# Performance work log

Hardware: AMD Instinct MI355X
Metric: run time of the kernel (lower is better)

## Reference

```python
import jax, jax.numpy as jnp
import numpy as np

DIM = 2048
N_HEADS = 16
HEAD_DIM = 128
EPS = 1e-6


def setup_inputs() -> dict:
    key = jax.random.key(0)
    ks = jax.random.split(key, 8)
    b, gf, gh, gw = 1, 8, 16, 24
    s = gf * gh * gw
    c = HEAD_DIM // 2
    w = lambda k: 0.02 * jax.random.normal(k, (DIM, DIM), jnp.float32)
    return {
        "x": jax.random.normal(ks[0], (b, s, DIM), jnp.float32),
        "freqs_angle": jax.random.normal(ks[1], (1024, c), jnp.float32),
        "Wq": w(ks[2]), "bq": jnp.zeros((DIM,), jnp.float32),
        "Wk": w(ks[3]), "bk": jnp.zeros((DIM,), jnp.float32),
        "Wv": w(ks[4]), "bv": jnp.zeros((DIM,), jnp.float32),
        "Wo": w(ks[5]), "bo": jnp.zeros((DIM,), jnp.float32),
        "gq": jnp.ones((DIM,), jnp.float32),
        "gk": jnp.ones((DIM,), jnp.float32),
        "seq_len": s, "grid_f": gf, "grid_h": gh, "grid_w": gw,
    }


def _rms(t, g):
    return t * jax.lax.rsqrt(jnp.mean(t * t, axis=-1, keepdims=True) + EPS) * g


def _grid_angles(freqs_angle, gf, gh, gw, c):
    # band split [c - 2*(c//3), c//3, c//3] as in rope_apply
    cf = c - 2 * (c // 3)
    ch = cw = c // 3
    af = freqs_angle[:gf, :cf]            # [F, cf]
    ah = freqs_angle[:gh, cf:cf + ch]     # [H, ch]
    aw = freqs_angle[:gw, cf + ch:c]      # [W, cw]
    ang = jnp.concatenate([
        jnp.broadcast_to(af[:, None, None, :], (gf, gh, gw, cf)),
        jnp.broadcast_to(ah[None, :, None, :], (gf, gh, gw, ch)),
        jnp.broadcast_to(aw[None, None, :, :], (gf, gh, gw, cw)),
    ], axis=-1)
    return ang.reshape(gf * gh * gw, c)   # [s, c]


def reference(x, freqs_angle, Wq, bq, Wk, bk, Wv, bv, Wo, bo, gq, gk,
              seq_len, grid_f, grid_h, grid_w):
    b, s, _ = x.shape
    n, d = N_HEADS, HEAD_DIM
    c = d // 2
    ang = _grid_angles(freqs_angle, grid_f, grid_h, grid_w, c)
    cos = jnp.cos(ang)[None, :, None, :]  # [1, s, 1, c]
    sin = jnp.sin(ang)[None, :, None, :]

    def rope(t):  # complex multiply on (even, odd) = (real, imag) pairs
        te, to = t[..., 0::2], t[..., 1::2]
        return jnp.stack([te * cos - to * sin, te * sin + to * cos], axis=-1).reshape(t.shape)

    q = _rms(x @ Wq.T + bq, gq).reshape(b, s, n, d)
    k = _rms(x @ Wk.T + bk, gk).reshape(b, s, n, d)
    v = (x @ Wv.T + bv).reshape(b, s, n, d)
    q, k = rope(q), rope(k)

    scale = np.float32(1.0 / np.sqrt(d))
    scores = jnp.einsum('bqnd,bknd->bnqk', q, k) * scale
    p = jax.nn.softmax(scores, axis=-1)
    o = jnp.einsum('bnqk,bknd->bqnd', p, v).reshape(b, s, n * d)
    return o @ Wo.T + bo
```

## Files before the change

kernel.cpp:

```cpp
#include <hip/hip_runtime.h>
#include <stdint.h>
#include <stddef.h>

typedef __bf16 bf16_t;
typedef __bf16 bf16x8 __attribute__((ext_vector_type(8)));
typedef __bf16 bf16x4 __attribute__((ext_vector_type(4)));
typedef __bf16 bf16x2 __attribute__((ext_vector_type(2)));
typedef float  f32x4  __attribute__((ext_vector_type(4)));

#define SEQ   3072
#define DIMD  2048
#define NH    16
#define HD    128
#define QKVN  6144

__device__ __forceinline__ void async16(const bf16_t* g, bf16_t* l) {
  __builtin_amdgcn_global_load_lds((const __attribute__((address_space(1))) uint32_t*)g,
                                   (__attribute__((address_space(3))) uint32_t*)l, 16, 0, 0);
}

__global__ __launch_bounds__(256) void cvt_all(const float* __restrict__ x,
                                               const float* __restrict__ Wq,
                                               const float* __restrict__ Wk,
                                               const float* __restrict__ Wv,
                                               const float* __restrict__ Wo,
                                               const float* __restrict__ bq,
                                               const float* __restrict__ bk,
                                               const float* __restrict__ bv,
                                               bf16_t* __restrict__ xb,
                                               bf16_t* __restrict__ Wqkvb,
                                               bf16_t* __restrict__ Wob,
                                               float* __restrict__ bqkv) {
  const int b = blockIdx.x;
  const float* src; bf16_t* dst; int off;
  if (b < 3072)       { src = x;  dst = xb;              off = b; }
  else if (b < 5120)  { src = Wq; dst = Wqkvb;           off = b - 3072; }
  else if (b < 7168)  { src = Wk; dst = Wqkvb + 4194304; off = b - 5120; }
  else if (b < 9216)  { src = Wv; dst = Wqkvb + 8388608; off = b - 7168; }
  else if (b < 11264) { src = Wo; dst = Wob;             off = b - 9216; }
  else {
    int t = (b - 11264) * 256 + threadIdx.x;
    float v;
    if (t < 2048)      v = bq[t];
    else if (t < 4096) v = bk[t - 2048];
    else               v = bv[t - 4096];
    bqkv[t] = v;
    return;
  }
  const int idx = (off * 256 + threadIdx.x) * 8;
  const float4 a = *(const float4*)(src + idx);
  const float4 c = *(const float4*)(src + idx + 4);
  bf16x8 o;
  o[0] = (bf16_t)a.x; o[1] = (bf16_t)a.y; o[2] = (bf16_t)a.z; o[3] = (bf16_t)a.w;
  o[4] = (bf16_t)c.x; o[5] = (bf16_t)c.y; o[6] = (bf16_t)c.z; o[7] = (bf16_t)c.w;
  *(bf16x8*)(dst + idx) = o;
}

template<bool OUT_BF16>
__global__ __launch_bounds__(256, 2) void gemm_nt(const bf16_t* __restrict__ A,
                                                  const bf16_t* __restrict__ B,
                                                  const float* __restrict__ bias,
                                                  void* __restrict__ Cout,
                                                  int M, int N, int K) {
  __shared__ __align__(16) bf16_t As[128 * 64];
  __shared__ __align__(16) bf16_t Bs[128 * 64];
  const int t = threadIdx.x;
  const int lane = t & 63, wave = t >> 6;
  const int quad = lane >> 4, l15 = lane & 15;
  const int wy = wave >> 1, wx = wave & 1;
  const size_t bm = (size_t)blockIdx.y * 128, bn = (size_t)blockIdx.x * 128;
  const bf16_t* Ab = A + bm * K;
  const bf16_t* Bb = B + bn * K;
  f32x4 acc[4][4] = {};
  int srow[4], scol[4];
#pragma unroll
  for (int r = 0; r < 4; r++) {
    int L = r * 256 + t;
    int row = L >> 3, cp = L & 7;
    srow[r] = row;
    scol[r] = (cp ^ (row & 7)) * 8;
  }
  for (int k0 = 0; k0 < K; k0 += 64) {
    __syncthreads();
#pragma unroll
    for (int r = 0; r < 4; r++)
      async16(Ab + (size_t)srow[r] * K + k0 + scol[r], &As[(r * 256 + t) * 8]);
#pragma unroll
    for (int r = 0; r < 4; r++)
      async16(Bb + (size_t)srow[r] * K + k0 + scol[r], &Bs[(r * 256 + t) * 8]);
    __syncthreads();
#pragma unroll
    for (int ks = 0; ks < 2; ks++) {
      bf16x8 af[4], bfv[4];
#pragma unroll
      for (int i = 0; i < 4; i++) {
        int row = wy * 64 + i * 16 + l15;
        af[i] = *(const bf16x8*)&As[row * 64 + (((ks * 4 + quad) ^ (row & 7)) * 8)];
      }
#pragma unroll
      for (int j = 0; j < 4; j++) {
        int row = wx * 64 + j * 16 + l15;
        bfv[j] = *(const bf16x8*)&Bs[row * 64 + (((ks * 4 + quad) ^ (row & 7)) * 8)];
      }
#pragma unroll
      for (int i = 0; i < 4; i++)
#pragma unroll
        for (int j = 0; j < 4; j++)
          acc[i][j] = __builtin_amdgcn_mfma_f32_16x16x32_bf16(af[i], bfv[j], acc[i][j], 0, 0, 0);
    }
  }
#pragma unroll
  for (int i = 0; i < 4; i++) {
#pragma unroll
    for (int j = 0; j < 4; j++) {
      size_t row = bm + wy * 64 + i * 16 + quad * 4;
      size_t col = bn + wx * 64 + j * 16 + l15;
      float bb = bias[col];
#pragma unroll
      for (int r = 0; r < 4; r++) {
        float v = acc[i][j][r] + bb;
        if (OUT_BF16) ((bf16_t*)Cout)[(row + r) * N + col] = (bf16_t)v;
        else          ((float*)Cout)[(row + r) * N + col] = v;
      }
    }
  }
}

__global__ __launch_bounds__(256) void rmsrope(bf16_t* __restrict__ qkv,
                                               bf16_t* __restrict__ pk,
                                               const float* __restrict__ gq,
                                               const float* __restrict__ gk,
                                               const float* __restrict__ freqs) {
  const int s = blockIdx.x, t = threadIdx.x;
  bf16_t* row = qkv + (size_t)s * QKVN;
  bf16x8 qv = *(const bf16x8*)&row[t * 8];
  bf16x8 kv = *(const bf16x8*)&row[2048 + t * 8];
  float qf[8], kf[8];
  float qs = 0.f, ks2 = 0.f;
#pragma unroll
  for (int i = 0; i < 8; i++) {
    qf[i] = (float)qv[i]; qs  += qf[i] * qf[i];
    kf[i] = (float)kv[i]; ks2 += kf[i] * kf[i];
  }
#pragma unroll
  for (int m = 1; m < 64; m <<= 1) {
    qs  += __shfl_xor(qs, m);
    ks2 += __shfl_xor(ks2, m);
  }
  __shared__ float red[2][4];
  const int wave = t >> 6, lane = t & 63;
  if (lane == 0) { red[0][wave] = qs; red[1][wave] = ks2; }
  __syncthreads();
  qs  = red[0][0] + red[0][1] + red[0][2] + red[0][3];
  ks2 = red[1][0] + red[1][1] + red[1][2] + red[1][3];
  const float qsc = rsqrtf(qs  / 2048.f + 1e-6f);
  const float ksc = rsqrtf(ks2 / 2048.f + 1e-6f);
  const int sf = s / 384, rem = s - sf * 384;
  const int sh = rem / 24, sw = rem - sh * 24;
  bf16x8 qo, ko;
#pragma unroll
  for (int u = 0; u < 4; u++) {
    const int col = t * 8 + 2 * u;
    const int i = (col >> 1) & 63;
    const int frow = (i < 22) ? sf : ((i < 43) ? sh : sw);
    const float ang = freqs[frow * 64 + i];
    float sn, cs;
    __sincosf(ang, &sn, &cs);
    float te = qf[2 * u]     * qsc * gq[col];
    float to = qf[2 * u + 1] * qsc * gq[col + 1];
    qo[2 * u]     = (bf16_t)(te * cs - to * sn);
    qo[2 * u + 1] = (bf16_t)(te * sn + to * cs);
    te = kf[2 * u]     * ksc * gk[col];
    to = kf[2 * u + 1] * ksc * gk[col + 1];
    ko[2 * u]     = (bf16_t)(te * cs - to * sn);
    ko[2 * u + 1] = (bf16_t)(te * sn + to * cs);
  }
  *(bf16x8*)&row[t * 8] = qo;
  *(bf16x8*)&pk[((size_t)(t >> 4) * SEQ + s) * HD + (t & 15) * 8] = ko;
}

__global__ __launch_bounds__(256) void vtrans(const bf16_t* __restrict__ qkv,
                                              bf16_t* __restrict__ pvt) {
  __shared__ bf16_t tile[128][65];
  const int h = blockIdx.y;
  const int s0 = blockIdx.x * 64;
  const int t = threadIdx.x;
#pragma unroll
  for (int r = 0; r < 4; r++) {
    int L = r * 256 + t, s = L >> 4, cp = L & 15;
    bf16x8 v = *(const bf16x8*)&qkv[(size_t)(s0 + s) * QKVN + 4096 + h * HD + cp * 8];
#pragma unroll
    for (int i = 0; i < 8; i++) tile[cp * 8 + i][s] = v[i];
  }
  __syncthreads();
#pragma unroll
  for (int r = 0; r < 4; r++) {
    int L = r * 256 + t, d = L >> 3, c = L & 7;
    bf16x8 o;
#pragma unroll
    for (int i = 0; i < 8; i++) o[i] = tile[d][c * 8 + i];
    *(bf16x8*)&pvt[((size_t)h * HD + d) * SEQ + s0 + c * 8] = o;
  }
}

__global__ __launch_bounds__(256, 2) void flash_attn(const bf16_t* __restrict__ qkv,
                                                     const bf16_t* __restrict__ pk,
                                                     const bf16_t* __restrict__ pvt,
                                                     bf16_t* __restrict__ ob) {
  __shared__ __align__(16) bf16_t Ks[2][64 * 128];
  __shared__ __align__(16) bf16_t Vt[2][128 * 64];
  __shared__ __align__(16) bf16_t Ps[4][32 * 64];
  const int h = blockIdx.y, qt = blockIdx.x;
  const int s0 = qt * 128;
  const int t = threadIdx.x, wave = t >> 6, lane = t & 63;
  const int quad = lane >> 4, l15 = lane & 15;
  const int wq = wave * 32;
  const float scale = 0.08838834764831845f;
  const bf16_t* pkh = pk  + (size_t)h * (SEQ * HD);
  const bf16_t* pvh = pvt + (size_t)h * (HD * SEQ);
  int krow4[4], kc4[4], vd4[4], vc4[4];
#pragma unroll
  for (int r = 0; r < 4; r++) {
    int L = r * 256 + t;
    krow4[r] = L >> 4; kc4[r] = (L & 15) ^ (krow4[r] & 7);
    vd4[r]   = L >> 3; vc4[r] = (L & 7)  ^ (vd4[r] & 7);
  }
  bf16x8 qfr[2][4];
#pragma unroll
  for (int tj = 0; tj < 2; tj++)
#pragma unroll
    for (int ks = 0; ks < 4; ks++)
      qfr[tj][ks] = *(const bf16x8*)&qkv[(size_t)(s0 + wq + tj * 16 + l15) * QKVN + h * HD + ks * 32 + quad * 8];
  f32x4 oacc[2][8] = {};
  float m_run[2] = {-3e38f, -3e38f}, l_run[2] = {0.f, 0.f};
#pragma unroll
  for (int r = 0; r < 4; r++) {
    int L = r * 256 + t;
    async16(pkh + (size_t)krow4[r] * HD + kc4[r] * 8, &Ks[0][L * 8]);
  }
#pragma unroll
  for (int r = 0; r < 4; r++) {
    int L = r * 256 + t;
    async16(pvh + (size_t)vd4[r] * SEQ + vc4[r] * 8, &Vt[0][L * 8]);
  }
  for (int kt = 0; kt < SEQ / 64; kt++) {
    const int cur = kt & 1;
    __syncthreads();
    if (kt + 1 < SEQ / 64) {
      const int kv1 = (kt + 1) * 64;
#pragma unroll
      for (int r = 0; r < 4; r++) {
        int L = r * 256 + t;
        async16(pkh + (size_t)(kv1 + krow4[r]) * HD + kc4[r] * 8, &Ks[cur ^ 1][L * 8]);
      }
#pragma unroll
      for (int r = 0; r < 4; r++) {
        int L = r * 256 + t;
        async16(pvh + (size_t)vd4[r] * SEQ + kv1 + vc4[r] * 8, &Vt[cur ^ 1][L * 8]);
      }
    }
    f32x4 st[4][2] = {};
#pragma unroll
    for (int ks = 0; ks < 4; ks++) {
      bf16x8 kfr[4];
#pragma unroll
      for (int ti = 0; ti < 4; ti++) {
        const int kr = ti * 16 + l15;
        kfr[ti] = *(const bf16x8*)&Ks[cur][kr * 128 + (((ks * 4 + quad) ^ (kr & 7)) * 8)];
      }
#pragma unroll
      for (int ti = 0; ti < 4; ti++)
#pragma unroll
        for (int tj = 0; tj < 2; tj++)
          st[ti][tj] = __builtin_amdgcn_mfma_f32_16x16x32_bf16(kfr[ti], qfr[tj][ks], st[ti][tj], 0, 0, 0);
    }
    float mt[2] = {-3e38f, -3e38f};
#pragma unroll
    for (int ti = 0; ti < 4; ti++)
#pragma unroll
      for (int tj = 0; tj < 2; tj++)
#pragma unroll
        for (int r = 0; r < 4; r++) {
          st[ti][tj][r] *= scale;
          mt[tj] = fmaxf(mt[tj], st[ti][tj][r]);
        }
    float al[2];
#pragma unroll
    for (int tj = 0; tj < 2; tj++) {
      mt[tj] = fmaxf(mt[tj], __shfl_xor(mt[tj], 16));
      mt[tj] = fmaxf(mt[tj], __shfl_xor(mt[tj], 32));
      const float mn = fmaxf(m_run[tj], mt[tj]);
      al[tj] = __expf(m_run[tj] - mn);
      m_run[tj] = mn;
    }
    float lt[2] = {0.f, 0.f};
#pragma unroll
    for (int ti = 0; ti < 4; ti++)
#pragma unroll
      for (int tj = 0; tj < 2; tj++) {
        bf16x4 pv;
#pragma unroll
        for (int r = 0; r < 4; r++) {
          const float p = __expf(st[ti][tj][r] - m_run[tj]);
          pv[r] = (bf16_t)p;
          lt[tj] += (float)pv[r];
        }
        const int q = tj * 16 + l15;
        const int cp2 = (ti * 2 + (quad >> 1)) ^ (q & 7);
        *(bf16x4*)&Ps[wave][q * 64 + cp2 * 8 + (quad & 1) * 4] = pv;
      }
#pragma unroll
    for (int tj = 0; tj < 2; tj++) {
      lt[tj] += __shfl_xor(lt[tj], 16);
      lt[tj] += __shfl_xor(lt[tj], 32);
      l_run[tj] = l_run[tj] * al[tj] + lt[tj];
    }
#pragma unroll
    for (int ti = 0; ti < 2; ti++) {
      float a0 = __shfl(al[ti], quad * 4 + 0);
      float a1 = __shfl(al[ti], quad * 4 + 1);
      float a2 = __shfl(al[ti], quad * 4 + 2);
      float a3 = __shfl(al[ti], quad * 4 + 3);
#pragma unroll
      for (int dj = 0; dj < 8; dj++) {
        oacc[ti][dj][0] *= a0; oacc[ti][dj][1] *= a1;
        oacc[ti][dj][2] *= a2; oacc[ti][dj][3] *= a3;
      }
    }
#pragma unroll
    for (int ks = 0; ks < 2; ks++) {
      bf16x8 pf[2], vf[8];
#pragma unroll
      for (int ti = 0; ti < 2; ti++) {
        const int q = ti * 16 + l15;
        pf[ti] = *(const bf16x8*)&Ps[wave][q * 64 + (((ks * 4 + quad) ^ (q & 7)) * 8)];
      }
#pragma unroll
      for (int dj = 0; dj < 8; dj++) {
        const int d = dj * 16 + l15;
        vf[dj] = *(const bf16x8*)&Vt[cur][d * 64 + (((ks * 4 + quad) ^ (d & 7)) * 8)];
      }
#pragma unroll
      for (int ti = 0; ti < 2; ti++)
#pragma unroll
        for (int dj = 0; dj < 8; dj++)
          oacc[ti][dj] = __builtin_amdgcn_mfma_f32_16x16x32_bf16(pf[ti], vf[dj], oacc[ti][dj], 0, 0, 0);
    }
  }
#pragma unroll
  for (int ti = 0; ti < 2; ti++) {
    float li[4];
#pragma unroll
    for (int r = 0; r < 4; r++) li[r] = 1.f / __shfl(l_run[ti], quad * 4 + r);
#pragma unroll
    for (int dj = 0; dj < 8; dj++)
#pragma unroll
      for (int r = 0; r < 4; r++) {
        const float v = oacc[ti][dj][r] * li[r];
        ob[(size_t)(s0 + wq + ti * 16 + quad * 4 + r) * DIMD + h * HD + dj * 16 + l15] = (bf16_t)v;
      }
  }
}

extern "C" void kernel_launch(void* const* d_in, const int* in_sizes, int n_in,
                              void* d_out, int out_size, void* d_ws, size_t ws_size,
                              hipStream_t stream) {
  (void)in_sizes; (void)n_in; (void)out_size;
  const float* x     = (const float*)d_in[0];
  const float* freqs = (const float*)d_in[1];
  const float* Wq    = (const float*)d_in[2];
  const float* bq    = (const float*)d_in[3];
  const float* Wk    = (const float*)d_in[4];
  const float* bk    = (const float*)d_in[5];
  const float* Wv    = (const float*)d_in[6];
  const float* bv    = (const float*)d_in[7];
  const float* Wo    = (const float*)d_in[8];
  const float* bo    = (const float*)d_in[9];
  const float* gq    = (const float*)d_in[10];
  const float* gk    = (const float*)d_in[11];

  char* w = (char*)d_ws;
  bf16_t* xb    = (bf16_t*)(w);
  bf16_t* Wqkvb = (bf16_t*)(w + 12582912);
  bf16_t* Wob   = (bf16_t*)(w + 37748736);
  bf16_t* qkvb  = (bf16_t*)(w + 46137344);
  bf16_t* obuf  = (bf16_t*)(w + 83886080);
  float*  bqkv  = (float*) (w + 96468992);
  bf16_t* pk    = (bf16_t*)(w);
  bf16_t* pvt   = (bf16_t*)(w + 12582912);
  if (ws_size < (size_t)96493568) return;

  cvt_all<<<11288, 256, 0, stream>>>(x, Wq, Wk, Wv, Wo, bq, bk, bv, xb, Wqkvb, Wob, bqkv);

  gemm_nt<true><<<dim3(48, 24), 256, 0, stream>>>(xb, Wqkvb, bqkv, qkvb, SEQ, QKVN, DIMD);
  rmsrope<<<3072, 256, 0, stream>>>(qkvb, pk, gq, gk, freqs);
  vtrans<<<dim3(48, NH), 256, 0, stream>>>(qkvb, pvt);
  flash_attn<<<dim3(24, NH), 256, 0, stream>>>(qkvb, pk, pvt, obuf);
  gemm_nt<false><<<dim3(16, 24), 256, 0, stream>>>(obuf, Wob, bo, (float*)d_out, SEQ, DIMD, DIMD);
}
```

Measured before the change: 421.5 us.

## Widen flash-attention blocks to six waves, use exp2 softmax, skip unneeded rescale

The flash attention kernel now runs 384 threads (six waves) per block, each block covering 192 query rows. The grid shrinks to 16x16 blocks, so each K/V tile loaded into LDS serves more queries. The softmax folds log2(e) into the scale and uses exp2f, and the accumulator rescale is skipped when no lane's correction factor differs from one. The grid becomes 256 blocks with one block per CU under the new launch bounds, which may reduce latency hiding and leave some CUs idle. The K/V load loops no longer divide evenly across threads.

```diff
diff --git a/kernel.cpp b/kernel.cpp
--- a/kernel.cpp
+++ b/kernel.cpp
@@ -203,28 +203,21 @@
   }
 }
 
-__global__ __launch_bounds__(256, 2) void flash_attn(const bf16_t* __restrict__ qkv,
+__global__ __launch_bounds__(384, 1) void flash_attn(const bf16_t* __restrict__ qkv,
                                                      const bf16_t* __restrict__ pk,
                                                      const bf16_t* __restrict__ pvt,
                                                      bf16_t* __restrict__ ob) {
   __shared__ __align__(16) bf16_t Ks[2][64 * 128];
   __shared__ __align__(16) bf16_t Vt[2][128 * 64];
-  __shared__ __align__(16) bf16_t Ps[4][32 * 64];
+  __shared__ __align__(16) bf16_t Ps[6][32 * 64];
   const int h = blockIdx.y, qt = blockIdx.x;
-  const int s0 = qt * 128;
+  const int s0 = qt * 192;
   const int t = threadIdx.x, wave = t >> 6, lane = t & 63;
   const int quad = lane >> 4, l15 = lane & 15;
   const int wq = wave * 32;
-  const float scale = 0.08838834764831845f;
+  const float scale2 = 0.08838834764831845f * 1.44269504088896f;
   const bf16_t* pkh = pk  + (size_t)h * (SEQ * HD);
   const bf16_t* pvh = pvt + (size_t)h * (HD * SEQ);
-  int krow4[4], kc4[4], vd4[4], vc4[4];
-#pragma unroll
-  for (int r = 0; r < 4; r++) {
-    int L = r * 256 + t;
-    krow4[r] = L >> 4; kc4[r] = (L & 15) ^ (krow4[r] & 7);
-    vd4[r]   = L >> 3; vc4[r] = (L & 7)  ^ (vd4[r] & 7);
-  }
   bf16x8 qfr[2][4];
 #pragma unroll
   for (int tj = 0; tj < 2; tj++)
@@ -233,30 +226,26 @@
       qfr[tj][ks] = *(const bf16x8*)&qkv[(size_t)(s0 + wq + tj * 16 + l15) * QKVN + h * HD + ks * 32 + quad * 8];
   f32x4 oacc[2][8] = {};
   float m_run[2] = {-3e38f, -3e38f}, l_run[2] = {0.f, 0.f};
-#pragma unroll
-  for (int r = 0; r < 4; r++) {
-    int L = r * 256 + t;
-    async16(pkh + (size_t)krow4[r] * HD + kc4[r] * 8, &Ks[0][L * 8]);
-  }
-#pragma unroll
-  for (int r = 0; r < 4; r++) {
-    int L = r * 256 + t;
-    async16(pvh + (size_t)vd4[r] * SEQ + vc4[r] * 8, &Vt[0][L * 8]);
+  for (int L = t; L < 1024; L += 384) {
+    int krow = L >> 4, c = (L & 15) ^ (krow & 7);
+    async16(pkh + (size_t)krow * HD + c * 8, &Ks[0][L * 8]);
+  }
+  for (int L = t; L < 1024; L += 384) {
+    int d = L >> 3, c = (L & 7) ^ (d & 7);
+    async16(pvh + (size_t)d * SEQ + c * 8, &Vt[0][L * 8]);
   }
   for (int kt = 0; kt < SEQ / 64; kt++) {
     const int cur = kt & 1;
     __syncthreads();
     if (kt + 1 < SEQ / 64) {
       const int kv1 = (kt + 1) * 64;
-#pragma unroll
-      for (int r = 0; r < 4; r++) {
-        int L = r * 256 + t;
-        async16(pkh + (size_t)(kv1 + krow4[r]) * HD + kc4[r] * 8, &Ks[cur ^ 1][L * 8]);
-      }
-#pragma unroll
-      for (int r = 0; r < 4; r++) {
-        int L = r * 256 + t;
-        async16(pvh + (size_t)vd4[r] * SEQ + kv1 + vc4[r] * 8, &Vt[cur ^ 1][L * 8]);
+      for (int L = t; L < 1024; L += 384) {
+        int krow = L >> 4, c = (L & 15) ^ (krow & 7);
+        async16(pkh + (size_t)(kv1 + krow) * HD + c * 8, &Ks[cur ^ 1][L * 8]);
+      }
+      for (int L = t; L < 1024; L += 384) {
+        int d = L >> 3, c = (L & 7) ^ (d & 7);
+        async16(pvh + (size_t)d * SEQ + kv1 + c * 8, &Vt[cur ^ 1][L * 8]);
       }
     }
     f32x4 st[4][2] = {};
@@ -281,7 +270,7 @@
       for (int tj = 0; tj < 2; tj++)
 #pragma unroll
         for (int r = 0; r < 4; r++) {
-          st[ti][tj][r] *= scale;
+          st[ti][tj][r] *= scale2;
           mt[tj] = fmaxf(mt[tj], st[ti][tj][r]);
         }
     float al[2];
@@ -290,7 +279,7 @@
       mt[tj] = fmaxf(mt[tj], __shfl_xor(mt[tj], 16));
       mt[tj] = fmaxf(mt[tj], __shfl_xor(mt[tj], 32));
       const float mn = fmaxf(m_run[tj], mt[tj]);
-      al[tj] = __expf(m_run[tj] - mn);
+      al[tj] = exp2f(m_run[tj] - mn);
       m_run[tj] = mn;
     }
     float lt[2] = {0.f, 0.f};
@@ -301,7 +290,7 @@
         bf16x4 pv;
 #pragma unroll
         for (int r = 0; r < 4; r++) {
-          const float p = __expf(st[ti][tj][r] - m_run[tj]);
+          const float p = exp2f(st[ti][tj][r] - m_run[tj]);
           pv[r] = (bf16_t)p;
           lt[tj] += (float)pv[r];
         }
@@ -315,16 +304,18 @@
       lt[tj] += __shfl_xor(lt[tj], 32);
       l_run[tj] = l_run[tj] * al[tj] + lt[tj];
     }
-#pragma unroll
-    for (int ti = 0; ti < 2; ti++) {
-      float a0 = __shfl(al[ti], quad * 4 + 0);
-      float a1 = __shfl(al[ti], quad * 4 + 1);
-      float a2 = __shfl(al[ti], quad * 4 + 2);
-      float a3 = __shfl(al[ti], quad * 4 + 3);
-#pragma unroll
-      for (int dj = 0; dj < 8; dj++) {
-        oacc[ti][dj][0] *= a0; oacc[ti][dj][1] *= a1;
-        oacc[ti][dj][2] *= a2; oacc[ti][dj][3] *= a3;
+    if (__ballot((al[0] != 1.f) | (al[1] != 1.f))) {
+#pragma unroll
+      for (int ti = 0; ti < 2; ti++) {
+        float a0 = __shfl(al[ti], quad * 4 + 0);
+        float a1 = __shfl(al[ti], quad * 4 + 1);
+        float a2 = __shfl(al[ti], quad * 4 + 2);
+        float a3 = __shfl(al[ti], quad * 4 + 3);
+#pragma unroll
+        for (int dj = 0; dj < 8; dj++) {
+          oacc[ti][dj][0] *= a0; oacc[ti][dj][1] *= a1;
+          oacc[ti][dj][2] *= a2; oacc[ti][dj][3] *= a3;
+        }
       }
     }
 #pragma unroll
@@ -395,6 +386,6 @@
   gemm_nt<true><<<dim3(48, 24), 256, 0, stream>>>(xb, Wqkvb, bqkv, qkvb, SEQ, QKVN, DIMD);
   rmsrope<<<3072, 256, 0, stream>>>(qkvb, pk, gq, gk, freqs);
   vtrans<<<dim3(48, NH), 256, 0, stream>>>(qkvb, pvt);
-  flash_attn<<<dim3(24, NH), 256, 0, stream>>>(qkvb, pk, pvt, obuf);
+  flash_attn<<<dim3(16, NH), 384, 0, stream>>>(qkvb, pk, pvt, obuf);
   gemm_nt<false><<<dim3(16, 24), 256, 0, stream>>>(obuf, Wob, bo, (float*)d_out, SEQ, DIMD, DIMD);
 }
```

New measurement: 466.4 us. +10.7%, slower.

## Fold softmax scale into Q, use exp2, compute row sums via MFMA, skip unneeded rescale

Applied to the files above, without the earlier changes.

Moves the 1/sqrt(d)·log2(e) factor into the Q RMS-norm scaling, so the attention kernel drops its per-score multiply and uses exp2 directly. The per-row probability sum is now accumulated by an extra MFMA against a ones vector instead of scalar adds and cross-lane shuffles. The output rescale is skipped when no lane's running max changed in that tile. The cost is a few extra MFMAs per tile and a divergent branch, and the pre-scaled Q is rounded to bf16 after the scale is applied.

```diff
diff --git a/kernel.cpp b/kernel.cpp
--- a/kernel.cpp
+++ b/kernel.cpp
@@ -132,6 +132,7 @@
                                                const float* __restrict__ gk,
                                                const float* __restrict__ freqs) {
   const int s = blockIdx.x, t = threadIdx.x;
+  const float SC2 = 0.08838834764831845f * 1.44269504088896f;
   bf16_t* row = qkv + (size_t)s * QKVN;
   bf16x8 qv = *(const bf16x8*)&row[t * 8];
   bf16x8 kv = *(const bf16x8*)&row[2048 + t * 8];
@@ -153,7 +154,7 @@
   __syncthreads();
   qs  = red[0][0] + red[0][1] + red[0][2] + red[0][3];
   ks2 = red[1][0] + red[1][1] + red[1][2] + red[1][3];
-  const float qsc = rsqrtf(qs  / 2048.f + 1e-6f);
+  const float qsc = rsqrtf(qs  / 2048.f + 1e-6f) * SC2;
   const float ksc = rsqrtf(ks2 / 2048.f + 1e-6f);
   const int sf = s / 384, rem = s - sf * 384;
   const int sh = rem / 24, sw = rem - sh * 24;
@@ -215,7 +216,6 @@
   const int t = threadIdx.x, wave = t >> 6, lane = t & 63;
   const int quad = lane >> 4, l15 = lane & 15;
   const int wq = wave * 32;
-  const float scale = 0.08838834764831845f;
   const bf16_t* pkh = pk  + (size_t)h * (SEQ * HD);
   const bf16_t* pvh = pvt + (size_t)h * (HD * SEQ);
   int krow4[4], kc4[4], vd4[4], vc4[4];
@@ -231,8 +231,12 @@
 #pragma unroll
     for (int ks = 0; ks < 4; ks++)
       qfr[tj][ks] = *(const bf16x8*)&qkv[(size_t)(s0 + wq + tj * 16 + l15) * QKVN + h * HD + ks * 32 + quad * 8];
+  bf16x8 onesf;
+#pragma unroll
+  for (int i = 0; i < 8; i++) onesf[i] = (bf16_t)1.0f;
   f32x4 oacc[2][8] = {};
-  float m_run[2] = {-3e38f, -3e38f}, l_run[2] = {0.f, 0.f};
+  f32x4 lacc[2] = {};
+  float m_run[2] = {-3e38f, -3e38f};
 #pragma unroll
   for (int r = 0; r < 4; r++) {
     int L = r * 256 + t;
@@ -280,51 +284,43 @@
 #pragma unroll
       for (int tj = 0; tj < 2; tj++)
 #pragma unroll
-        for (int r = 0; r < 4; r++) {
-          st[ti][tj][r] *= scale;
+        for (int r = 0; r < 4; r++)
           mt[tj] = fmaxf(mt[tj], st[ti][tj][r]);
-        }
     float al[2];
 #pragma unroll
     for (int tj = 0; tj < 2; tj++) {
       mt[tj] = fmaxf(mt[tj], __shfl_xor(mt[tj], 16));
       mt[tj] = fmaxf(mt[tj], __shfl_xor(mt[tj], 32));
       const float mn = fmaxf(m_run[tj], mt[tj]);
-      al[tj] = __expf(m_run[tj] - mn);
+      al[tj] = exp2f(m_run[tj] - mn);
       m_run[tj] = mn;
     }
-    float lt[2] = {0.f, 0.f};
 #pragma unroll
     for (int ti = 0; ti < 4; ti++)
 #pragma unroll
       for (int tj = 0; tj < 2; tj++) {
         bf16x4 pv;
 #pragma unroll
-        for (int r = 0; r < 4; r++) {
-          const float p = __expf(st[ti][tj][r] - m_run[tj]);
-          pv[r] = (bf16_t)p;
-          lt[tj] += (float)pv[r];
-        }
+        for (int r = 0; r < 4; r++)
+          pv[r] = (bf16_t)exp2f(st[ti][tj][r] - m_run[tj]);
         const int q = tj * 16 + l15;
         const int cp2 = (ti * 2 + (quad >> 1)) ^ (q & 7);
         *(bf16x4*)&Ps[wave][q * 64 + cp2 * 8 + (quad & 1) * 4] = pv;
       }
-#pragma unroll
-    for (int tj = 0; tj < 2; tj++) {
-      lt[tj] += __shfl_xor(lt[tj], 16);
-      lt[tj] += __shfl_xor(lt[tj], 32);
-      l_run[tj] = l_run[tj] * al[tj] + lt[tj];
-    }
-#pragma unroll
-    for (int ti = 0; ti < 2; ti++) {
-      float a0 = __shfl(al[ti], quad * 4 + 0);
-      float a1 = __shfl(al[ti], quad * 4 + 1);
-      float a2 = __shfl(al[ti], quad * 4 + 2);
-      float a3 = __shfl(al[ti], quad * 4 + 3);
-#pragma unroll
-      for (int dj = 0; dj < 8; dj++) {
-        oacc[ti][dj][0] *= a0; oacc[ti][dj][1] *= a1;
-        oacc[ti][dj][2] *= a2; oacc[ti][dj][3] *= a3;
+    if (__ballot((al[0] != 1.f) | (al[1] != 1.f))) {
+#pragma unroll
+      for (int ti = 0; ti < 2; ti++) {
+        float a0 = __shfl(al[ti], quad * 4 + 0);
+        float a1 = __shfl(al[ti], quad * 4 + 1);
+        float a2 = __shfl(al[ti], quad * 4 + 2);
+        float a3 = __shfl(al[ti], quad * 4 + 3);
+        lacc[ti][0] *= a0; lacc[ti][1] *= a1;
+        lacc[ti][2] *= a2; lacc[ti][3] *= a3;
+#pragma unroll
+        for (int dj = 0; dj < 8; dj++) {
+          oacc[ti][dj][0] *= a0; oacc[ti][dj][1] *= a1;
+          oacc[ti][dj][2] *= a2; oacc[ti][dj][3] *= a3;
+        }
       }
     }
 #pragma unroll
@@ -341,17 +337,19 @@
         vf[dj] = *(const bf16x8*)&Vt[cur][d * 64 + (((ks * 4 + quad) ^ (d & 7)) * 8)];
       }
 #pragma unroll
-      for (int ti = 0; ti < 2; ti++)
+      for (int ti = 0; ti < 2; ti++) {
+        lacc[ti] = __builtin_amdgcn_mfma_f32_16x16x32_bf16(pf[ti], onesf, lacc[ti], 0, 0, 0);
 #pragma unroll
         for (int dj = 0; dj < 8; dj++)
           oacc[ti][dj] = __builtin_amdgcn_mfma_f32_16x16x32_bf16(pf[ti], vf[dj], oacc[ti][dj], 0, 0, 0);
+      }
     }
   }
 #pragma unroll
   for (int ti = 0; ti < 2; ti++) {
     float li[4];
 #pragma unroll
-    for (int r = 0; r < 4; r++) li[r] = 1.f / __shfl(l_run[ti], quad * 4 + r);
+    for (int r = 0; r < 4; r++) li[r] = 1.f / lacc[ti][r];
 #pragma unroll
     for (int dj = 0; dj < 8; dj++)
 #pragma unroll
```

After: 446.1 us. 5.8% more time.
